# Optimization experiments

Measured on AMD Instinct MI355X. Metric: run time of the kernel, lower is better.

The kernel has to match this reference:

```python
import jax, jax.numpy as jnp
import numpy as np

B, NQ, NK, D, H = 4, 2048, 2048, 1024, 16
DH = D // H
SCALE = DH ** -0.5


def setup_inputs() -> dict:
    key = jax.random.key(0)
    ks = jax.random.split(key, 8)
    s = 0.02
    return {
        "x_q": jax.random.normal(ks[0], (B, NQ, D), dtype=jnp.float32),
        "x_kv": jax.random.normal(ks[1], (B, NK, D), dtype=jnp.float32),
        "Wq": jax.random.normal(ks[2], (D, D), dtype=jnp.float32) * s,
        "bq": jnp.zeros((D,), dtype=jnp.float32),
        "Wkv": jax.random.normal(ks[3], (D, 2 * D), dtype=jnp.float32) * s,
        "bkv": jnp.zeros((2 * D,), dtype=jnp.float32),
        "Wp": jax.random.normal(ks[4], (D, D), dtype=jnp.float32) * s,
        "bp": jnp.zeros((D,), dtype=jnp.float32),
    }


def reference(x_q, x_kv, Wq, bq, Wkv, bkv, Wp, bp):
    # q: [B, H, Nq, Dh]
    q = (x_q @ Wq + bq).reshape(B, NQ, H, DH).transpose(0, 2, 1, 3)
    kv = (x_kv @ Wkv + bkv).reshape(B, NK, 2, H, DH)
    k = kv[:, :, 0].transpose(0, 2, 1, 3)  # [B, H, Nk, Dh]
    v = kv[:, :, 1].transpose(0, 2, 1, 3)  # [B, H, Nk, Dh]
    attn = jnp.einsum("bhqd,bhkd->bhqk", q, k) * SCALE  # [B, H, Nq, Nk]
    attn = jax.nn.softmax(attn, axis=-1)
    out = jnp.einsum("bhqk,bhkd->bhqd", attn, v)  # [B, H, Nq, Dh]
    out = out.transpose(0, 2, 1, 3).reshape(B, NQ, D)
    return jnp.nan_to_num(x_q + out @ Wp + bp)
```

## Files before the change

kernel.cpp:

```cpp
#include <hip/hip_runtime.h>
#include <hip/hip_bf16.h>

#define B_   4
#define NQ_  2048
#define NK_  2048
#define D_   1024
#define H_   16
#define DH_  64
#define SCALE_ 0.125f

typedef __attribute__((ext_vector_type(8))) __bf16 bf16x8;
typedef __attribute__((ext_vector_type(4))) float  f32x4;

typedef const __attribute__((address_space(1))) unsigned int* gas1p;
typedef __attribute__((address_space(3))) unsigned int*       las3p;

__device__ __forceinline__ f32x4 mfma16(bf16x8 a, bf16x8 b, f32x4 c) {
  return __builtin_amdgcn_mfma_f32_16x16x32_bf16(a, b, c, 0, 0, 0);
}
__device__ __forceinline__ void gload_lds16(const void* g, void* l) {
  __builtin_amdgcn_global_load_lds((gas1p)g, (las3p)l, 16, 0, 0);
}
__device__ __forceinline__ float nn_(float x) {
  if (__builtin_isnan(x)) return 0.0f;
  if (__builtin_isinf(x)) return x > 0.f ? 3.402823466e38f : -3.402823466e38f;
  return x;
}
__device__ __forceinline__ float exp2_(float x) {
#if __has_builtin(__builtin_amdgcn_exp2f)
  return __builtin_amdgcn_exp2f(x);
#else
  return __expf(x * 0.69314718056f);
#endif
}

__global__ __launch_bounds__(256) void cvt_bf16_k(const float* __restrict__ s,
                                                  __bf16* __restrict__ d, int n) {
  int i = (blockIdx.x * blockDim.x + threadIdx.x) << 2;
  if (i >= n) return;
  float4 v = *(const float4*)(s + i);
  __bf16 o[4] __attribute__((aligned(8))) = {(__bf16)v.x, (__bf16)v.y, (__bf16)v.z, (__bf16)v.w};
  *(uint2*)(d + i) = *(uint2*)o;
}

__global__ __launch_bounds__(256) void transpose_cvt_k(const float* __restrict__ src,
                                                       __bf16* __restrict__ dst,
                                                       int K, int N, float scale) {
  __shared__ float t[32][33];
  int n0 = blockIdx.x * 32, k0 = blockIdx.y * 32;
  int x = threadIdx.x, y0 = threadIdx.y;
  for (int yy = y0; yy < 32; yy += 8)
    t[yy][x] = src[(size_t)(k0 + yy) * N + n0 + x];
  __syncthreads();
  for (int yy = y0; yy < 32; yy += 8)
    dst[(size_t)(n0 + yy) * K + k0 + x] = (__bf16)(t[x][yy] * scale);
}

template <bool OUT_BF16, bool RES>
__global__ __launch_bounds__(512, 4) void gemm3p_k(const __bf16* __restrict__ A,
                                                   const __bf16* __restrict__ Bt,
                                                   const float* __restrict__ bias, float bscale,
                                                   const float* __restrict__ res,
                                                   void* __restrict__ out,
                                                   int M, int N, int K) {
  constexpr int BM = 256, BN = 128, BK = 32;
  __shared__ __attribute__((aligned(16))) __bf16 Al[3][BM * BK];
  __shared__ __attribute__((aligned(16))) __bf16 Bl[3][BN * BK];
  const int tid = threadIdx.x, lane = tid & 63, wid = tid >> 6;
  const int wr = wid >> 1, wc = wid & 1;
  const int g = lane >> 4, lr = lane & 15;
  const int m0 = blockIdx.y * BM, n0 = blockIdx.x * BN;

  const int ca1 = tid + 512;
  const int rowA0 = tid >> 2, rowA1 = ca1 >> 2, rowB = tid >> 2;
  const __bf16* aSrc0 = A + (size_t)(m0 + rowA0) * K + (((tid & 3) ^ (rowA0 & 3)) << 3);
  const __bf16* aSrc1 = A + (size_t)(m0 + rowA1) * K + (((ca1 & 3) ^ (rowA1 & 3)) << 3);
  const __bf16* bSrc  = Bt + (size_t)(n0 + rowB) * K + (((tid & 3) ^ (rowB & 3)) << 3);
  char* aDst0 = (char*)&Al[0][0] + (tid << 4);
  char* aDst1 = (char*)&Al[0][0] + (ca1 << 4);
  char* bDst  = (char*)&Bl[0][0] + (tid << 4);

  const int swz = (lr & 3) << 4;
  int offA[4], offB[4];
#pragma unroll
  for (int m = 0; m < 4; m++) offA[m] = (wr * 64 + m * 16 + lr) * 64 + ((g * 16) ^ swz);
#pragma unroll
  for (int n = 0; n < 4; n++) offB[n] = (wc * 64 + n * 16 + lr) * 64 + ((g * 16) ^ swz);

  const f32x4 zero4 = {0.f, 0.f, 0.f, 0.f};
  f32x4 acc[4][4];
#pragma unroll
  for (int m = 0; m < 4; m++)
#pragma unroll
    for (int n = 0; n < 4; n++) acc[m][n] = zero4;

  gload_lds16(aSrc0, aDst0); gload_lds16(aSrc1, aDst1); gload_lds16(bSrc, bDst);
  gload_lds16(aSrc0 + BK, aDst0 + 16384); gload_lds16(aSrc1 + BK, aDst1 + 16384);
  gload_lds16(bSrc + BK, bDst + 8192);
  asm volatile("s_waitcnt vmcnt(3)" ::: "memory");
  __builtin_amdgcn_s_barrier();

  const int KT = K / BK;
  int cb = 0, b2 = 2;
  for (int t = 0; t < KT; ++t) {
    const char* Ab = (const char*)&Al[0][0] + cb * 16384;
    const char* Bb = (const char*)&Bl[0][0] + cb * 8192;
    bf16x8 af[4], bv[4];
#pragma unroll
    for (int m = 0; m < 4; m++) af[m] = *(const bf16x8*)(Ab + offA[m]);
#pragma unroll
    for (int n = 0; n < 4; n++) bv[n] = *(const bf16x8*)(Bb + offB[n]);
    if (t < KT - 2) {
      const int k2 = (t + 2) * BK;
      gload_lds16(aSrc0 + k2, aDst0 + b2 * 16384);
      gload_lds16(aSrc1 + k2, aDst1 + b2 * 16384);
      gload_lds16(bSrc + k2, bDst + b2 * 8192);
    }
    asm volatile("s_waitcnt lgkmcnt(0)" ::: "memory");
    __builtin_amdgcn_sched_barrier(0);
    __builtin_amdgcn_s_setprio(1);
#pragma unroll
    for (int m = 0; m < 4; m++)
#pragma unroll
      for (int n = 0; n < 4; n++) acc[m][n] = mfma16(af[m], bv[n], acc[m][n]);
    __builtin_amdgcn_s_setprio(0);
    if (t < KT - 2)       asm volatile("s_waitcnt vmcnt(3)" ::: "memory");
    else if (t == KT - 2) asm volatile("s_waitcnt vmcnt(0)" ::: "memory");
    if (t < KT - 1) __builtin_amdgcn_s_barrier();
    cb = (cb == 2) ? 0 : cb + 1;
    b2 = (b2 == 2) ? 0 : b2 + 1;
  }

#pragma unroll
  for (int Mi = 0; Mi < 4; ++Mi) {
    int row = m0 + wr * 64 + Mi * 16 + g * 4;
#pragma unroll
    for (int Ni = 0; Ni < 4; ++Ni) {
      int col = n0 + wc * 64 + Ni * 16 + lr;
      float bvv = bias[col] * bscale;
#pragma unroll
      for (int r = 0; r < 4; ++r) {
        size_t idx = (size_t)(row + r) * N + col;
        float v = acc[Mi][Ni][r] + bvv;
        if (RES) v = nn_(v + res[idx]);
        if (OUT_BF16) ((__bf16*)out)[idx] = (__bf16)v;
        else          ((float*)out)[idx] = v;
      }
    }
  }
}

__global__ __launch_bounds__(256) void reorder_v_k(const __bf16* __restrict__ kv,
                                                   __bf16* __restrict__ vt) {
  __shared__ __attribute__((aligned(16))) __bf16 t[64][72];
  int bh = blockIdx.y, b = bh >> 4, h = bh & 15;
  int kk0 = blockIdx.x * 64;
  int tid = threadIdx.x;
#pragma unroll
  for (int i = 0; i < 2; i++) {
    int c = tid + i * 256;
    int kk = c >> 3, dc = c & 7;
    const __bf16* src = kv + (size_t)(b * NK_ + kk0 + kk) * 2048 + 1024 + h * 64 + dc * 8;
    *(float4*)&t[kk][dc * 8] = *(const float4*)src;
  }
  __syncthreads();
#pragma unroll
  for (int i = 0; i < 2; i++) {
    int c = tid + i * 256;
    int d = c >> 3, gch = c & 7;
    int s = gch ^ (d & 7);
    __bf16 tmp[8] __attribute__((aligned(16)));
#pragma unroll
    for (int j = 0; j < 8; j++) tmp[j] = t[s * 8 + j][d];
    __bf16* dst = vt + ((size_t)bh * 64 + d) * (size_t)NK_ + kk0 + gch * 8;
    *(float4*)dst = *(float4*)tmp;
  }
}

__global__ __launch_bounds__(256) void attn_k(const __bf16* __restrict__ Qg,
                                              const __bf16* __restrict__ KVg,
                                              const __bf16* __restrict__ Vt,
                                              __bf16* __restrict__ AO) {
  __shared__ __attribute__((aligned(16))) __bf16 Kt[2][64 * 64];
  __shared__ __attribute__((aligned(16))) __bf16 Vl[2][64 * 64];
  __shared__ __attribute__((aligned(16))) __bf16 Pl[4][16 * 64];
  const int tid = threadIdx.x, lane = tid & 63, wid = tid >> 6;
  const int g = lane >> 4, lr = lane & 15;
  const int bid = blockIdx.x;
  const int bh = bid & 63, b = bh >> 4, h = bh & 15;
  const int qbase = (bid >> 6) * 64 + wid * 16;

  bf16x8 qf[2];
  {
    const __bf16* qp = Qg + ((size_t)(b * NQ_ + qbase + lr)) * 1024 + h * 64 + g * 8;
    qf[0] = *(const bf16x8*)qp;
    qf[1] = *(const bf16x8*)(qp + 32);
  }

  const f32x4 zero4 = {0.f, 0.f, 0.f, 0.f};
  f32x4 po[4];
#pragma unroll
  for (int df = 0; df < 4; df++) po[df] = zero4;
  float m2 = -1e30f, l = 0.f;

  char* pw = (char*)&Pl[wid][0];
  const int swz = (lr & 7) << 4;
  int wa[4], ra[2];
#pragma unroll
  for (int n = 0; n < 4; n++) wa[n] = lr * 128 + ((n * 32 + g * 8) ^ swz);
#pragma unroll
  for (int ks = 0; ks < 2; ks++) ra[ks] = lr * 128 + ((ks * 64 + g * 16) ^ swz);

  const int kkw = wid * 16 + (lane >> 3);
  const int cc = lane & 7;
  const __bf16* Ksrc = KVg + (size_t)b * NK_ * 2048 + h * 64;
  const __bf16* Vsrc = Vt + (size_t)bh * 64 * (size_t)NK_;

#define STAGE_(bi, kv0)                                                              \
  {                                                                                  \
    _Pragma("unroll") for (int i = 0; i < 2; i++) {                                  \
      int kk = kkw + i * 8;                                                          \
      gload_lds16(Ksrc + (size_t)((kv0) + kk) * 2048 + ((cc ^ (kk & 7)) << 3),       \
                  (char*)&Kt[bi][0] + wid * 2048 + i * 1024);                        \
      gload_lds16(Vsrc + (size_t)kk * NK_ + (kv0) + (cc << 3),                       \
                  (char*)&Vl[bi][0] + wid * 2048 + i * 1024);                        \
    }                                                                                \
  }

  int cur = 0;
  STAGE_(0, 0);

  for (int t = 0; t < NK_ / 64; ++t) {
    const int kv0 = t << 6;
    if (t < NK_ / 64 - 1) {
      STAGE_(cur ^ 1, kv0 + 64);
      asm volatile("s_waitcnt vmcnt(4)" ::: "memory");
    } else {
      asm volatile("s_waitcnt vmcnt(0)" ::: "memory");
    }
    asm volatile("s_barrier" ::: "memory");

    const char* Kb = (const char*)&Kt[cur][0];
    const char* Vb = (const char*)&Vl[cur][0];

    f32x4 sa[4];
    __builtin_amdgcn_s_setprio(1);
#pragma unroll
    for (int n = 0; n < 4; n++) {
      sa[n] = zero4;
      int kk = n * 16 + lr;
#pragma unroll
      for (int ds = 0; ds < 2; ds++) {
        bf16x8 kf = *(const bf16x8*)(Kb + kk * 128 + ((ds * 64 + g * 16) ^ ((kk & 7) << 4)));
        sa[n] = mfma16(kf, qf[ds], sa[n]);
      }
    }
    __builtin_amdgcn_s_setprio(0);

    float mx = -1e30f;
#pragma unroll
    for (int n = 0; n < 4; n++)
#pragma unroll
      for (int r = 0; r < 4; r++) mx = fmaxf(mx, sa[n][r]);
    mx = fmaxf(mx, __shfl_xor(mx, 16));
    mx = fmaxf(mx, __shfl_xor(mx, 32));

    if (__any(mx > m2 + 11.0f)) {
      float mn = fmaxf(m2, mx);
      float alpha = exp2_(m2 - mn);
      m2 = mn;
      l *= alpha;
#pragma unroll
      for (int r = 0; r < 4; r++) {
        float ar = __shfl(alpha, g * 4 + r);
#pragma unroll
        for (int df = 0; df < 4; df++) po[df][r] *= ar;
      }
    }

    float rs = 0.f;
#pragma unroll
    for (int n = 0; n < 4; n++) {
      union { __bf16 hh[4]; uint2 u; } qd;
#pragma unroll
      for (int r = 0; r < 4; r++) {
        float p = exp2_(sa[n][r] - m2);
        rs += p;
        qd.hh[r] = (__bf16)p;
      }
      *(uint2*)(pw + wa[n]) = qd.u;
    }
    rs += __shfl_xor(rs, 16);
    rs += __shfl_xor(rs, 32);
    l += rs;

    asm volatile("s_waitcnt lgkmcnt(0)" ::: "memory");

    bf16x8 pa[2];
#pragma unroll
    for (int ks = 0; ks < 2; ks++) pa[ks] = *(const bf16x8*)(pw + ra[ks]);

    __builtin_amdgcn_s_setprio(1);
#pragma unroll
    for (int df = 0; df < 4; df++) {
      int d = df * 16 + lr;
#pragma unroll
      for (int ks = 0; ks < 2; ks++) {
        bf16x8 vf = *(const bf16x8*)(Vb + d * 128 + ((ks * 64 + g * 16) ^ ((d & 7) << 4)));
        po[df] = mfma16(pa[ks], vf, po[df]);
      }
    }
    __builtin_amdgcn_s_setprio(0);

    asm volatile("s_barrier" ::: "memory");
    cur ^= 1;
  }

  float inv = 1.0f / l;
#pragma unroll
  for (int r = 0; r < 4; r++) {
    float ir = __shfl(inv, g * 4 + r);
    size_t row = (size_t)(b * NQ_ + qbase + g * 4 + r);
#pragma unroll
    for (int df = 0; df < 4; df++)
      AO[row * 1024 + h * 64 + df * 16 + lr] = (__bf16)(po[df][r] * ir);
  }
#undef STAGE_
}

extern "C" void kernel_launch(void* const* d_in, const int* in_sizes, int n_in,
                              void* d_out, int out_size, void* d_ws, size_t ws_size,
                              hipStream_t stream) {
  (void)in_sizes; (void)n_in; (void)out_size; (void)ws_size;
  const float* x_q  = (const float*)d_in[0];
  const float* x_kv = (const float*)d_in[1];
  const float* Wq   = (const float*)d_in[2];
  const float* bq   = (const float*)d_in[3];
  const float* Wkv  = (const float*)d_in[4];
  const float* bkv  = (const float*)d_in[5];
  const float* Wp   = (const float*)d_in[6];
  const float* bp   = (const float*)d_in[7];

  char* w = (char*)d_ws;
  __bf16* xq_bf  = (__bf16*)w; w += (size_t)8388608 * 2;
  __bf16* xkv_bf = (__bf16*)w; w += (size_t)8388608 * 2;
  __bf16* Wq_t   = (__bf16*)w; w += (size_t)1048576 * 2;
  __bf16* Wkv_t  = (__bf16*)w; w += (size_t)2097152 * 2;
  __bf16* Wp_t   = (__bf16*)w; w += (size_t)1048576 * 2;
  __bf16* Q_bf   = (__bf16*)w; w += (size_t)8388608 * 2;
  __bf16* KV_bf  = (__bf16*)w; w += (size_t)16777216 * 2;
  __bf16* Vt     = (__bf16*)w; w += (size_t)8388608 * 2;
  __bf16* AO     = (__bf16*)w; w += (size_t)8388608 * 2;

  const float C2 = SCALE_ * 1.44269504089f;

  cvt_bf16_k<<<8192, 256, 0, stream>>>(x_q, xq_bf, 8388608);
  cvt_bf16_k<<<8192, 256, 0, stream>>>(x_kv, xkv_bf, 8388608);
  transpose_cvt_k<<<dim3(32, 32), dim3(32, 8), 0, stream>>>(Wq, Wq_t, 1024, 1024, C2);
  transpose_cvt_k<<<dim3(64, 32), dim3(32, 8), 0, stream>>>(Wkv, Wkv_t, 1024, 2048, 1.0f);
  transpose_cvt_k<<<dim3(32, 32), dim3(32, 8), 0, stream>>>(Wp, Wp_t, 1024, 1024, 1.0f);

  gemm3p_k<true, false><<<dim3(8, 32), 512, 0, stream>>>(xq_bf, Wq_t, bq, C2, nullptr, Q_bf, 8192, 1024, 1024);
  gemm3p_k<true, false><<<dim3(16, 32), 512, 0, stream>>>(xkv_bf, Wkv_t, bkv, 1.0f, nullptr, KV_bf, 8192, 2048, 1024);
  reorder_v_k<<<dim3(32, 64), 256, 0, stream>>>(KV_bf, Vt);
  attn_k<<<2048, 256, 0, stream>>>(Q_bf, KV_bf, Vt, AO);
  gemm3p_k<false, true><<<dim3(8, 32), 512, 0, stream>>>(AO, Wp_t, bp, 1.0f, x_q, d_out, 8192, 1024, 1024);
}
```

Before: 390.5 us.

## Unroll attention loop by two with static LDS buffers and incremental pointers

Restructures the flash-attention KV loop into a two-way unrolled body with compile-time buffer indices and pointer-increment staging, removing per-iteration address recomputation and dynamic buffer selection. It also drops the explicit lgkmcnt(0) waits in both the GEMM and attention loops, leaving LDS ordering to the compiler, and uses a three-input max chain for the row max. Dropping the manual waits relies on compiler-inserted waits for correctness and may change instruction scheduling.

```diff
diff --git a/kernel.cpp b/kernel.cpp
--- a/kernel.cpp
+++ b/kernel.cpp
@@ -32,6 +32,9 @@
 #else
   return __expf(x * 0.69314718056f);
 #endif
+}
+__device__ __forceinline__ float fmax3_(float a, float b, float c) {
+  return fmaxf(fmaxf(a, b), c);
 }
 
 __global__ __launch_bounds__(256) void cvt_bf16_k(const float* __restrict__ s,
@@ -116,8 +119,6 @@
       gload_lds16(aSrc1 + k2, aDst1 + b2 * 16384);
       gload_lds16(bSrc + k2, bDst + b2 * 8192);
     }
-    asm volatile("s_waitcnt lgkmcnt(0)" ::: "memory");
-    __builtin_amdgcn_sched_barrier(0);
     __builtin_amdgcn_s_setprio(1);
 #pragma unroll
     for (int m = 0; m < 4; m++)
@@ -204,116 +205,111 @@
   float m2 = -1e30f, l = 0.f;
 
   char* pw = (char*)&Pl[wid][0];
-  const int swz = (lr & 7) << 4;
+  const int pswz = (lr & 7) << 4;
   int wa[4], ra[2];
 #pragma unroll
-  for (int n = 0; n < 4; n++) wa[n] = lr * 128 + ((n * 32 + g * 8) ^ swz);
-#pragma unroll
-  for (int ks = 0; ks < 2; ks++) ra[ks] = lr * 128 + ((ks * 64 + g * 16) ^ swz);
-
-  const int kkw = wid * 16 + (lane >> 3);
+  for (int n = 0; n < 4; n++) wa[n] = lr * 128 + ((n * 32 + g * 8) ^ pswz);
+#pragma unroll
+  for (int ks = 0; ks < 2; ks++) ra[ks] = lr * 128 + ((ks * 64 + g * 16) ^ pswz);
+
+  const int kk = wid * 16 + (lane >> 3);
   const int cc = lane & 7;
-  const __bf16* Ksrc = KVg + (size_t)b * NK_ * 2048 + h * 64;
-  const __bf16* Vsrc = Vt + (size_t)bh * 64 * (size_t)NK_;
-
-#define STAGE_(bi, kv0)                                                              \
-  {                                                                                  \
-    _Pragma("unroll") for (int i = 0; i < 2; i++) {                                  \
-      int kk = kkw + i * 8;                                                          \
-      gload_lds16(Ksrc + (size_t)((kv0) + kk) * 2048 + ((cc ^ (kk & 7)) << 3),       \
-                  (char*)&Kt[bi][0] + wid * 2048 + i * 1024);                        \
-      gload_lds16(Vsrc + (size_t)kk * NK_ + (kv0) + (cc << 3),                       \
-                  (char*)&Vl[bi][0] + wid * 2048 + i * 1024);                        \
-    }                                                                                \
-  }
-
-  int cur = 0;
-  STAGE_(0, 0);
-
-  for (int t = 0; t < NK_ / 64; ++t) {
-    const int kv0 = t << 6;
-    if (t < NK_ / 64 - 1) {
-      STAGE_(cur ^ 1, kv0 + 64);
+  const __bf16* kp0 = KVg + (size_t)b * NK_ * 2048 + h * 64 + (size_t)kk * 2048 + ((cc ^ (kk & 7)) << 3);
+  const __bf16* kp1 = kp0 + 8 * 2048;
+  const __bf16* vp0 = Vt + (size_t)bh * 64 * (size_t)NK_ + (size_t)kk * NK_ + (cc << 3);
+  const __bf16* vp1 = vp0 + 8 * NK_;
+  char* kd0 = (char*)&Kt[0][0] + wid * 2048;
+  char* vd0 = (char*)&Vl[0][0] + wid * 2048;
+
+#define STAGE_(bi)                                             \
+  {                                                            \
+    gload_lds16(kp0, kd0 + (bi) * 8192);                       \
+    gload_lds16(kp1, kd0 + (bi) * 8192 + 1024);                \
+    gload_lds16(vp0, vd0 + (bi) * 8192);                       \
+    gload_lds16(vp1, vd0 + (bi) * 8192 + 1024);                \
+    kp0 += 64 * 2048; kp1 += 64 * 2048; vp0 += 64; vp1 += 64;  \
+  }
+
+#define BODY_(bi)                                                                              \
+  {                                                                                            \
+    const char* Kb = (const char*)&Kt[bi][0];                                                  \
+    const char* Vb = (const char*)&Vl[bi][0];                                                  \
+    f32x4 sa[4];                                                                               \
+    __builtin_amdgcn_s_setprio(1);                                                             \
+    _Pragma("unroll") for (int n = 0; n < 4; n++) {                                            \
+      sa[n] = zero4;                                                                           \
+      int kr = n * 16 + lr;                                                                    \
+      _Pragma("unroll") for (int ds = 0; ds < 2; ds++) {                                       \
+        bf16x8 kf = *(const bf16x8*)(Kb + kr * 128 + ((ds * 64 + g * 16) ^ ((kr & 7) << 4)));  \
+        sa[n] = mfma16(kf, qf[ds], sa[n]);                                                     \
+      }                                                                                        \
+    }                                                                                          \
+    __builtin_amdgcn_s_setprio(0);                                                             \
+    float mx = fmax3_(sa[0][0], sa[0][1], sa[0][2]);                                           \
+    mx = fmax3_(mx, sa[0][3], sa[1][0]);                                                       \
+    mx = fmax3_(mx, sa[1][1], sa[1][2]);                                                       \
+    mx = fmax3_(mx, sa[1][3], sa[2][0]);                                                       \
+    mx = fmax3_(mx, sa[2][1], sa[2][2]);                                                       \
+    mx = fmax3_(mx, sa[2][3], sa[3][0]);                                                       \
+    mx = fmax3_(mx, sa[3][1], sa[3][2]);                                                       \
+    mx = fmaxf(mx, sa[3][3]);                                                                  \
+    mx = fmaxf(mx, __shfl_xor(mx, 16));                                                        \
+    mx = fmaxf(mx, __shfl_xor(mx, 32));                                                        \
+    if (__any(mx > m2 + 11.0f)) {                                                              \
+      float mn = fmaxf(m2, mx);                                                                \
+      float alpha = exp2_(m2 - mn);                                                            \
+      m2 = mn;                                                                                 \
+      l *= alpha;                                                                              \
+      _Pragma("unroll") for (int r = 0; r < 4; r++) {                                          \
+        float ar = __shfl(alpha, g * 4 + r);                                                   \
+        _Pragma("unroll") for (int df = 0; df < 4; df++) po[df][r] *= ar;                      \
+      }                                                                                        \
+    }                                                                                          \
+    float rs = 0.f;                                                                            \
+    _Pragma("unroll") for (int n = 0; n < 4; n++) {                                            \
+      union { __bf16 hh[4]; uint2 u; } qd;                                                     \
+      _Pragma("unroll") for (int r = 0; r < 4; r++) {                                          \
+        float p = exp2_(sa[n][r] - m2);                                                        \
+        rs += p;                                                                               \
+        qd.hh[r] = (__bf16)p;                                                                  \
+      }                                                                                        \
+      *(uint2*)(pw + wa[n]) = qd.u;                                                            \
+    }                                                                                          \
+    rs += __shfl_xor(rs, 16);                                                                  \
+    rs += __shfl_xor(rs, 32);                                                                  \
+    l += rs;                                                                                   \
+    bf16x8 pa[2];                                                                              \
+    _Pragma("unroll") for (int ks = 0; ks < 2; ks++)                                           \
+      pa[ks] = *(const bf16x8*)(pw + ra[ks]);                                                  \
+    __builtin_amdgcn_s_setprio(1);                                                             \
+    _Pragma("unroll") for (int df = 0; df < 4; df++) {                                         \
+      int d = df * 16 + lr;                                                                    \
+      _Pragma("unroll") for (int ks = 0; ks < 2; ks++) {                                       \
+        bf16x8 vf = *(const bf16x8*)(Vb + d * 128 + ((ks * 64 + g * 16) ^ ((d & 7) << 4)));    \
+        po[df] = mfma16(pa[ks], vf, po[df]);                                                   \
+      }                                                                                        \
+    }                                                                                          \
+    __builtin_amdgcn_s_setprio(0);                                                             \
+  }
+
+  STAGE_(0);
+
+#pragma unroll 1
+  for (int it = 0; it < 16; ++it) {
+    STAGE_(1);
+    asm volatile("s_waitcnt vmcnt(4)" ::: "memory");
+    asm volatile("s_barrier" ::: "memory");
+    BODY_(0);
+    asm volatile("s_barrier" ::: "memory");
+    if (it < 15) {
+      STAGE_(0);
       asm volatile("s_waitcnt vmcnt(4)" ::: "memory");
     } else {
       asm volatile("s_waitcnt vmcnt(0)" ::: "memory");
     }
     asm volatile("s_barrier" ::: "memory");
-
-    const char* Kb = (const char*)&Kt[cur][0];
-    const char* Vb = (const char*)&Vl[cur][0];
-
-    f32x4 sa[4];
-    __builtin_amdgcn_s_setprio(1);
-#pragma unroll
-    for (int n = 0; n < 4; n++) {
-      sa[n] = zero4;
-      int kk = n * 16 + lr;
-#pragma unroll
-      for (int ds = 0; ds < 2; ds++) {
-        bf16x8 kf = *(const bf16x8*)(Kb + kk * 128 + ((ds * 64 + g * 16) ^ ((kk & 7) << 4)));
-        sa[n] = mfma16(kf, qf[ds], sa[n]);
-      }
-    }
-    __builtin_amdgcn_s_setprio(0);
-
-    float mx = -1e30f;
-#pragma unroll
-    for (int n = 0; n < 4; n++)
-#pragma unroll
-      for (int r = 0; r < 4; r++) mx = fmaxf(mx, sa[n][r]);
-    mx = fmaxf(mx, __shfl_xor(mx, 16));
-    mx = fmaxf(mx, __shfl_xor(mx, 32));
-
-    if (__any(mx > m2 + 11.0f)) {
-      float mn = fmaxf(m2, mx);
-      float alpha = exp2_(m2 - mn);
-      m2 = mn;
-      l *= alpha;
-#pragma unroll
-      for (int r = 0; r < 4; r++) {
-        float ar = __shfl(alpha, g * 4 + r);
-#pragma unroll
-        for (int df = 0; df < 4; df++) po[df][r] *= ar;
-      }
-    }
-
-    float rs = 0.f;
-#pragma unroll
-    for (int n = 0; n < 4; n++) {
-      union { __bf16 hh[4]; uint2 u; } qd;
-#pragma unroll
-      for (int r = 0; r < 4; r++) {
-        float p = exp2_(sa[n][r] - m2);
-        rs += p;
-        qd.hh[r] = (__bf16)p;
-      }
-      *(uint2*)(pw + wa[n]) = qd.u;
-    }
-    rs += __shfl_xor(rs, 16);
-    rs += __shfl_xor(rs, 32);
-    l += rs;
-
-    asm volatile("s_waitcnt lgkmcnt(0)" ::: "memory");
-
-    bf16x8 pa[2];
-#pragma unroll
-    for (int ks = 0; ks < 2; ks++) pa[ks] = *(const bf16x8*)(pw + ra[ks]);
-
-    __builtin_amdgcn_s_setprio(1);
-#pragma unroll
-    for (int df = 0; df < 4; df++) {
-      int d = df * 16 + lr;
-#pragma unroll
-      for (int ks = 0; ks < 2; ks++) {
-        bf16x8 vf = *(const bf16x8*)(Vb + d * 128 + ((ks * 64 + g * 16) ^ ((d & 7) << 4)));
-        po[df] = mfma16(pa[ks], vf, po[df]);
-      }
-    }
-    __builtin_amdgcn_s_setprio(0);
-
+    BODY_(1);
     asm volatile("s_barrier" ::: "memory");
-    cur ^= 1;
   }
 
   float inv = 1.0f / l;
@@ -326,6 +322,7 @@
       AO[row * 1024 + h * 64 + df * 16 + lr] = (__bf16)(po[df][r] * ir);
   }
 #undef STAGE_
+#undef BODY_
 }
 
 extern "C" void kernel_launch(void* const* d_in, const int* in_sizes, int n_in,
```

After: 389.9 us. Within noise of the previous version (-0.2%).
